# Performance work log

Measured on AMD Instinct MI355X. Metric: run time of the kernel, lower is better.

The kernel has to match this reference:

```python
import jax, jax.numpy as jnp
import numpy as np

B = 524288          # batch of independent 6x6 matching problems
ITERS = 100         # sinkhorn iterations (module training mode uses num_iterations)
EPS = 1e-12


def setup_inputs() -> dict:
    key = jax.random.key(0)
    ks = jax.random.split(key, 6)
    margins = jax.random.uniform(ks[0], (B, 12), jnp.float32, 0.1, 1.0)

    def glorot(k, shape):
        fan = shape[0] + shape[-1]
        return jax.random.normal(k, shape, jnp.float32) * np.float32(np.sqrt(2.0 / fan))

    W1 = glorot(ks[1], (12, 32)); b1 = jnp.zeros((32,), jnp.float32)
    W2 = glorot(ks[2], (32, 16)); b2 = jnp.zeros((16,), jnp.float32)
    W3 = glorot(ks[3], (16, 18)); b3 = jnp.zeros((18,), jnp.float32)
    # tau: log-linear positive map from an 8-vector of positives to a 6x6 matrix
    Wtau = jax.random.normal(ks[4], (8, 6, 6), jnp.float32) * 0.1
    return dict(margins=margins, W1=W1, b1=b1, W2=W2, b2=b2, W3=W3, b3=b3, Wtau=Wtau)


def _squash(x, low=0.02, high=0.98):
    return low + (high - low) * jax.nn.sigmoid(x)


def _forward(margins, W1, b1, W2, b2, W3, b3, Wtau, iters):
    M, F = margins[:, 0:6], margins[:, 6:12]
    # tiny MLP producing per-sample parameters
    h = jax.nn.relu(margins @ W1 + b1)
    h = jax.nn.relu(h @ W2 + b2)
    pars = h @ W3 + b3                                    # [B, 18]
    # tau(exp(pars[:,0:8])): log-linear positive 6x6 matrix, vectorized over batch
    A = jnp.exp(jnp.einsum('bk,kij->bij', pars[:, 0:8], Wtau))   # [B, 6, 6]
    ones = jnp.ones((margins.shape[0], 1), margins.dtype)
    shm0 = jnp.concatenate([_squash(pars[:, 9:11]), ones,
                            _squash(pars[:, 11:13]), ones], axis=1)   # [B, 6]
    shf0 = jnp.concatenate([_squash(pars[:, 13:15]), ones,
                            _squash(pars[:, 15:17]), ones], axis=1)   # [B, 6]
    V = jnp.exp(pars[:, -1])                                          # [B]
    mucm0, muc0f = M * shm0, F * shf0       # row / col margins for sinkhorn
    mum0, mu0f = M * (1.0 - shm0), F * (1.0 - shf0)
    rm = mucm0[:, :, None]                  # [B, 6, 1]
    cm = muc0f[:, None, :]                  # [B, 1, 6]

    def step(A, _):
        A = A * (rm / (A.sum(axis=2, keepdims=True) + EPS))
        A = A * (cm / (A.sum(axis=1, keepdims=True) + EPS))
        return A, None

    A, _ = jax.lax.scan(step, A, None, length=iters)
    top = jnp.concatenate([A, mum0[:, :, None]], axis=2)                       # [B, 6, 7]
    bot = jnp.concatenate([mu0f[:, None, :],
                           jnp.zeros((margins.shape[0], 1, 1), margins.dtype)], axis=2)  # [B, 1, 7]
    mus = jnp.concatenate([top, bot], axis=1)                                  # [B, 7, 7]
    return mus, V


def reference(margins, W1, b1, W2, b2, W3, b3, Wtau):
    return _forward(margins, W1, b1, W2, b2, W3, b3, Wtau, ITERS)
```

## Files before the change

### kernel.cpp

```cpp
#include <hip/hip_runtime.h>
#include <math.h>

#define MAX_ITERS 100
#define EPS 1e-12f
#define TOL 3e-5f

__device__ __forceinline__ float fast_rcp(float x) {
    return __builtin_amdgcn_rcpf(x);
}

__device__ __forceinline__ float squash(float x) {
    return 0.02f + 0.96f * fast_rcp(1.0f + __expf(-x));
}

__global__ __launch_bounds__(256, 2) void sinkhorn_km_kernel(
    const float* __restrict__ margins,
    const float* __restrict__ W1, const float* __restrict__ b1,
    const float* __restrict__ W2, const float* __restrict__ b2,
    const float* __restrict__ W3, const float* __restrict__ b3,
    const float* __restrict__ Wtau,
    float* __restrict__ out, int B)
{
    __shared__ float side[256 * 13];
    const int tid = threadIdx.x;
    const int b = blockIdx.x * 256 + tid;
    if (b >= B) return;
    float* sd = side + tid * 13;

    const float4* mp = (const float4*)(margins + (size_t)b * 12);
    float4 m0 = mp[0], m1 = mp[1], m2 = mp[2];
    float mar[12] = {m0.x, m0.y, m0.z, m0.w,
                     m1.x, m1.y, m1.z, m1.w,
                     m2.x, m2.y, m2.z, m2.w};

    float h1[32];
#pragma unroll
    for (int o = 0; o < 32; ++o) {
        float acc = b1[o];
#pragma unroll
        for (int i = 0; i < 12; ++i) acc = fmaf(mar[i], W1[i * 32 + o], acc);
        h1[o] = acc > 0.0f ? acc : 0.0f;
    }
    float h2[16];
#pragma unroll
    for (int o = 0; o < 16; ++o) {
        float acc = b2[o];
#pragma unroll
        for (int i = 0; i < 32; ++i) acc = fmaf(h1[i], W2[i * 16 + o], acc);
        h2[o] = acc > 0.0f ? acc : 0.0f;
    }
    float pars[18];
#pragma unroll
    for (int o = 0; o < 18; ++o) {
        float acc = b3[o];
#pragma unroll
        for (int i = 0; i < 16; ++i) acc = fmaf(h2[i], W3[i * 18 + o], acc);
        pars[o] = acc;
    }

    float shm[6] = {squash(pars[9]),  squash(pars[10]), 1.0f,
                    squash(pars[11]), squash(pars[12]), 1.0f};
    float shf[6] = {squash(pars[13]), squash(pars[14]), 1.0f,
                    squash(pars[15]), squash(pars[16]), 1.0f};
    float rm[6], cm[6];
#pragma unroll
    for (int j = 0; j < 6; ++j) {
        float Mj = mar[j], Fj = mar[6 + j];
        rm[j] = Mj * shm[j];
        cm[j] = Fj * shf[j];
        sd[j]     = Mj - rm[j];
        sd[6 + j] = Fj - cm[j];
    }
    sd[12] = __expf(pars[17]);

    float A[36];
#pragma unroll
    for (int e = 0; e < 36; ++e) {
        float acc = 0.0f;
#pragma unroll
        for (int k = 0; k < 8; ++k) acc = fmaf(pars[k], Wtau[k * 36 + e], acc);
        A[e] = __expf(acc);
    }

    for (int t = 0; t < MAX_ITERS; ++t) {
        float f[6];
#pragma unroll
        for (int i = 0; i < 6; ++i) {
            float s = 0.0f;
#pragma unroll
            for (int j = 0; j < 6; ++j) s += A[i * 6 + j];
            f[i] = rm[i] * fast_rcp(s + EPS);
#pragma unroll
            for (int j = 0; j < 6; ++j) A[i * 6 + j] *= f[i];
        }
#pragma unroll
        for (int j = 0; j < 6; ++j) {
            float s = 0.0f;
#pragma unroll
            for (int i = 0; i < 6; ++i) s += A[i * 6 + j];
            float g = cm[j] * fast_rcp(s + EPS);
#pragma unroll
            for (int i = 0; i < 6; ++i) A[i * 6 + j] *= g;
        }
        float fmax = fmaxf(fmaxf(fmaxf(f[0], f[1]), fmaxf(f[2], f[3])),
                           fmaxf(f[4], f[5]));
        float fmin = fminf(fminf(fminf(f[0], f[1]), fminf(f[2], f[3])),
                           fminf(f[4], f[5]));
        if (__all(fmax - fmin <= TOL * fmax)) break;
    }

    float* o = out + (size_t)b * 49;
#pragma unroll
    for (int i = 0; i < 6; ++i) {
#pragma unroll
        for (int j = 0; j < 6; ++j) o[i * 7 + j] = A[i * 6 + j];
        o[i * 7 + 6] = sd[i];
    }
#pragma unroll
    for (int j = 0; j < 6; ++j) o[42 + j] = sd[6 + j];
    o[48] = 0.0f;
    out[(size_t)B * 49 + b] = sd[12];
}

extern "C" void kernel_launch(void* const* d_in, const int* in_sizes, int n_in,
                              void* d_out, int out_size, void* d_ws, size_t ws_size,
                              hipStream_t stream) {
    const float* margins = (const float*)d_in[0];
    const float* W1   = (const float*)d_in[1];
    const float* b1   = (const float*)d_in[2];
    const float* W2   = (const float*)d_in[3];
    const float* b2   = (const float*)d_in[4];
    const float* W3   = (const float*)d_in[5];
    const float* b3   = (const float*)d_in[6];
    const float* Wtau = (const float*)d_in[7];
    const int B = in_sizes[0] / 12;

    dim3 block(256);
    dim3 grid((B + 255) / 256);
    hipLaunchKernelGGL(sinkhorn_km_kernel, grid, block, 0, stream,
                       margins, W1, b1, W2, b2, W3, b3, Wtau,
                       (float*)d_out, B);
}
```

Baseline: 182.4 us.

## Stage per-block outputs in LDS and write coalesced float4 tiles

```diff
diff --git a/kernel.cpp b/kernel.cpp
--- a/kernel.cpp
+++ b/kernel.cpp
@@ -13,7 +13,7 @@
     return 0.02f + 0.96f * fast_rcp(1.0f + __expf(-x));
 }
 
-__global__ __launch_bounds__(256, 2) void sinkhorn_km_kernel(
+__global__ __launch_bounds__(64, 4) void sinkhorn_km_kernel(
     const float* __restrict__ margins,
     const float* __restrict__ W1, const float* __restrict__ b1,
     const float* __restrict__ W2, const float* __restrict__ b2,
@@ -21,17 +21,24 @@
     const float* __restrict__ Wtau,
     float* __restrict__ out, int B)
 {
-    __shared__ float side[256 * 13];
-    const int tid = threadIdx.x;
-    const int b = blockIdx.x * 256 + tid;
-    if (b >= B) return;
-    float* sd = side + tid * 13;
+    __shared__ __align__(16) float tile[64 * 49];
+    const int l  = threadIdx.x;
+    const int wg = blockIdx.x;
+    const int b  = wg * 64 + l;
+    const bool valid = (b < B);
+    float* my = tile + l * 49;
 
-    const float4* mp = (const float4*)(margins + (size_t)b * 12);
-    float4 m0 = mp[0], m1 = mp[1], m2 = mp[2];
-    float mar[12] = {m0.x, m0.y, m0.z, m0.w,
-                     m1.x, m1.y, m1.z, m1.w,
-                     m2.x, m2.y, m2.z, m2.w};
+    float mar[12];
+    if (valid) {
+        const float4* mp = (const float4*)(margins + (size_t)b * 12);
+        float4 m0 = mp[0], m1 = mp[1], m2 = mp[2];
+        mar[0] = m0.x; mar[1] = m0.y; mar[2]  = m0.z; mar[3]  = m0.w;
+        mar[4] = m1.x; mar[5] = m1.y; mar[6]  = m1.z; mar[7]  = m1.w;
+        mar[8] = m2.x; mar[9] = m2.y; mar[10] = m2.z; mar[11] = m2.w;
+    } else {
+#pragma unroll
+        for (int i = 0; i < 12; ++i) mar[i] = 0.5f;
+    }
 
     float h1[32];
 #pragma unroll
@@ -62,16 +69,18 @@
                     squash(pars[11]), squash(pars[12]), 1.0f};
     float shf[6] = {squash(pars[13]), squash(pars[14]), 1.0f,
                     squash(pars[15]), squash(pars[16]), 1.0f};
+    const float V = __expf(pars[17]);
+
     float rm[6], cm[6];
 #pragma unroll
     for (int j = 0; j < 6; ++j) {
         float Mj = mar[j], Fj = mar[6 + j];
         rm[j] = Mj * shm[j];
         cm[j] = Fj * shf[j];
-        sd[j]     = Mj - rm[j];
-        sd[6 + j] = Fj - cm[j];
+        my[j * 7 + 6] = Mj - rm[j];
+        my[42 + j]    = Fj - cm[j];
     }
-    sd[12] = __expf(pars[17]);
+    my[48] = 0.0f;
 
     float A[36];
 #pragma unroll
@@ -109,17 +118,26 @@
         if (__all(fmax - fmin <= TOL * fmax)) break;
     }
 
-    float* o = out + (size_t)b * 49;
 #pragma unroll
-    for (int i = 0; i < 6; ++i) {
+    for (int i = 0; i < 6; ++i)
 #pragma unroll
-        for (int j = 0; j < 6; ++j) o[i * 7 + j] = A[i * 6 + j];
-        o[i * 7 + 6] = sd[i];
+        for (int j = 0; j < 6; ++j) my[i * 7 + j] = A[i * 6 + j];
+
+    __syncthreads();
+
+    if (wg * 64 + 64 <= B) {
+        float4* gdst = (float4*)(out + (size_t)wg * (64 * 49));
+        const float4* lsrc = (const float4*)tile;
+#pragma unroll
+        for (int k = 0; k < 12; ++k) gdst[k * 64 + l] = lsrc[k * 64 + l];
+        if (l < 16) gdst[768 + l] = lsrc[768 + l];
+    } else if (valid) {
+        float* o = out + (size_t)b * 49;
+#pragma unroll
+        for (int k = 0; k < 49; ++k) o[k] = my[k];
     }
-#pragma unroll
-    for (int j = 0; j < 6; ++j) o[42 + j] = sd[6 + j];
-    o[48] = 0.0f;
-    out[(size_t)B * 49 + b] = sd[12];
+
+    if (valid) out[(size_t)B * 49 + b] = V;
 }
 
 extern "C" void kernel_launch(void* const* d_in, const int* in_sizes, int n_in,
@@ -135,8 +153,8 @@
     const float* Wtau = (const float*)d_in[7];
     const int B = in_sizes[0] / 12;
 
-    dim3 block(256);
-    dim3 grid((B + 255) / 256);
+    dim3 block(64);
+    dim3 grid((B + 63) / 64);
     hipLaunchKernelGGL(sinkhorn_km_kernel, grid, block, 0, stream,
                        margins, W1, b1, W2, b2, W3, b3, Wtau,
                        (float*)d_out, B);
```

Result: slower. 208.1 us (+14.1%).
